# Optimization experiments

Hardware: AMD Instinct MI355X
Metric: run time of the kernel (lower is better)

## Reference

```python
import jax, jax.numpy as jnp
import numpy as np

D_MODEL = 256
NHEAD = 8
AGG = 4
NPE = (832.0, 832.0, 832.0, 832.0)
LAYER_NAMES = ['self', 'cross'] * 4


def layer_norm(x, g, b, eps=1e-5):
    mu = x.mean(-1, keepdims=True)
    var = ((x - mu) ** 2).mean(-1, keepdims=True)
    return (x - mu) * jax.lax.rsqrt(var + eps) * g + b


def rope_tables(h, w, d_model=D_MODEL):
    # i/j positions start at 1 (torch cumsum of ones); npe train/test scaling
    i = (jnp.arange(1, h + 1, dtype=jnp.float32) * (NPE[0] / NPE[2]))[:, None, None]
    j = (jnp.arange(1, w + 1, dtype=jnp.float32) * (NPE[1] / NPE[3]))[None, :, None]
    d4 = d_model // 4
    div = jnp.exp(jnp.arange(d4, dtype=jnp.float32) * (-np.log(10000.0) / d4))

    def interleave(a, bb):
        a = jnp.broadcast_to(a, (h, w, d4))
        bb = jnp.broadcast_to(bb, (h, w, d4))
        return jnp.stack([a, bb], -1).reshape(h, w, 2 * d4)

    sin = interleave(jnp.sin(i * div), jnp.sin(j * div))
    cos = interleave(jnp.cos(i * div), jnp.cos(j * div))
    return jnp.repeat(sin, 2, axis=-1), jnp.repeat(cos, 2, axis=-1)  # [h,w,d_model]


def rotate_half(x):
    xp = x.reshape(*x.shape[:-1], -1, 2)
    return jnp.stack([-xp[..., 1], xp[..., 0]], -1).reshape(*x.shape)


def apply_rope(x, sin, cos):  # x: [b,h,w,c]
    return x * cos + rotate_half(x) * sin


def encoder_layer(x, source, p, use_rope):
    bs, C, H0, W0 = x.shape
    # depthwise-conv aggregation of query features (stride=kernel=AGG, no bias)
    q = jax.lax.conv_general_dilated(
        x, p['agg_w'], (AGG, AGG), 'VALID',
        dimension_numbers=('NCHW', 'OIHW', 'NCHW'), feature_group_count=C)
    q = layer_norm(q.transpose(0, 2, 3, 1), p['ln1_g'], p['ln1_b'])  # [b,h,w,C]
    # max-pool aggregation of source features
    s = jax.lax.reduce_window(source, -jnp.inf, jax.lax.max,
                              (1, 1, AGG, AGG), (1, 1, AGG, AGG), 'VALID')
    s = layer_norm(s.transpose(0, 2, 3, 1), p['ln1_g'], p['ln1_b'])
    query = q @ p['qw']
    key = s @ p['kw']
    value = s @ p['vw']
    if use_rope:
        sin_q, cos_q = rope_tables(query.shape[1], query.shape[2])
        query = apply_rope(query, sin_q, cos_q)
        sin_k, cos_k = rope_tables(key.shape[1], key.shape[2])
        key = apply_rope(key, sin_k, cos_k)
    L = query.shape[1] * query.shape[2]
    S = key.shape[1] * key.shape[2]
    dh = C // NHEAD
    qh = query.reshape(bs, L, NHEAD, dh)
    kh = key.reshape(bs, S, NHEAD, dh)
    vh = value.reshape(bs, S, NHEAD, dh)
    scores = jnp.einsum('blhd,bshd->bhls', qh, kh) / jnp.asarray(dh, qh.dtype) ** 0.5
    attn = jax.nn.softmax(scores, axis=-1)
    m = jnp.einsum('bhls,bshd->blhd', attn, vh).reshape(bs, L, C)
    m = m @ p['mw']  # merge
    m = m.reshape(bs, H0 // AGG, W0 // AGG, C).transpose(0, 3, 1, 2)
    # bilinear upsample x4, align_corners=False (half-pixel, matches jax.image)
    m = jax.image.resize(m, (bs, C, H0, W0), method='bilinear')
    cat = jnp.concatenate([x, m], axis=1).transpose(0, 2, 3, 1)  # [b,H,W,2C]
    h1 = cat @ p['w1']
    h1 = jnp.where(h1 >= 0, h1, 0.01 * h1)  # LeakyReLU
    out = layer_norm(h1 @ p['w2'], p['ln2_g'], p['ln2_b']).transpose(0, 3, 1, 2)
    return x + out


def _forward(feat0, feat1, params):
    for i, name in enumerate(LAYER_NAMES):
        p = {k: v[i] for k, v in params.items()}
        if name == 'self':
            feat0 = encoder_layer(feat0, feat0, p, use_rope=True)
            feat1 = encoder_layer(feat1, feat1, p, use_rope=True)
        else:
            feat0 = encoder_layer(feat0, feat1, p, use_rope=False)
            feat1 = encoder_layer(feat1, feat0, p, use_rope=False)
    return feat0, feat1


def setup_inputs() -> dict:
    key = jax.random.key(0)
    ks = jax.random.split(key, 10)
    C = D_MODEL
    NL = len(LAYER_NAMES)

    def xavier(k, shape, fan_in, fan_out):
        return jax.random.normal(k, shape, jnp.float32) * np.sqrt(2.0 / (fan_in + fan_out))

    return {
        'feat0': jax.random.normal(ks[0], (2, C, 96, 96), jnp.float32),
        'feat1': jax.random.normal(ks[1], (2, C, 96, 96), jnp.float32),
        'agg_w': jax.random.normal(ks[2], (NL, C, 1, AGG, AGG), jnp.float32) * 0.1,
        'qw': xavier(ks[3], (NL, C, C), C, C),
        'kw': xavier(ks[4], (NL, C, C), C, C),
        'vw': xavier(ks[5], (NL, C, C), C, C),
        'mw': xavier(ks[6], (NL, C, C), C, C),
        'w1': xavier(ks[7], (NL, 2 * C, 2 * C), 2 * C, 2 * C),
        'w2': xavier(ks[8], (NL, 2 * C, C), 2 * C, C),
        'ln1_g': jnp.ones((NL, C), jnp.float32),
        'ln1_b': jnp.zeros((NL, C), jnp.float32),
        'ln2_g': jnp.ones((NL, C), jnp.float32),
        'ln2_b': jnp.zeros((NL, C), jnp.float32),
    }


def reference(feat0, feat1, agg_w, qw, kw, vw, mw, w1, w2, ln1_g, ln1_b, ln2_g, ln2_b):
    params = dict(agg_w=agg_w, qw=qw, kw=kw, vw=vw, mw=mw, w1=w1, w2=w2,
                  ln1_g=ln1_g, ln1_b=ln1_b, ln2_g=ln2_g, ln2_b=ln2_b)
    return _forward(feat0, feat1, params)
```

## Files before the change

kernel.cpp:

```cpp
#include <hip/hip_runtime.h>
#include <math.h>

constexpr int BSZ = 2;
constexpr int CH  = 256;
constexpr int IH  = 96, IW = 96;
constexpr int HSS = 24, WSS = 24;
constexpr int SL  = HSS * WSS;
constexpr int NHD = 8, DHD = 32;
constexpr int CH2 = 512;
constexpr int PIX = IH * IW;
constexpr int MFFN = BSZ * PIX;
constexpr long FEATN = (long)BSZ * PIX * CH;

typedef __attribute__((ext_vector_type(8))) short bf16x8;
typedef __attribute__((ext_vector_type(4))) float f32x4;
typedef _Float16 f16;
typedef __attribute__((ext_vector_type(8))) _Float16 f16x8;
typedef __attribute__((ext_vector_type(4))) _Float16 f16x4;


__device__ inline unsigned short f2bf(float f) {
  unsigned u = __float_as_uint(f);
  u += 0x7FFFu + ((u >> 16) & 1u);
  return (unsigned short)(u >> 16);
}
__device__ inline float bf2f(unsigned short u) {
  return __uint_as_float((unsigned)u << 16);
}

__device__ inline void gload16(const void* g, void* l) {
  __builtin_amdgcn_global_load_lds(
      (const __attribute__((address_space(1))) unsigned int*)g,
      (__attribute__((address_space(3))) unsigned int*)l, 16, 0, 0);
}

__global__ __launch_bounds__(256) void k_in_tr(const float* __restrict__ in,
                                               float* __restrict__ out,
                                               unsigned short* __restrict__ outb) {
  __shared__ float t[32][33];
  const int b = blockIdx.z;
  const int p0 = blockIdx.x * 32, c0 = blockIdx.y * 32;
  const int tx = threadIdx.x & 31, ty = threadIdx.x >> 5;
#pragma unroll
  for (int r = 0; r < 4; ++r)
    t[tx][ty + r * 8] = in[((long)b * CH + c0 + ty + r * 8) * PIX + p0 + tx];
  __syncthreads();
#pragma unroll
  for (int r = 0; r < 4; ++r) {
    float v = t[ty + r * 8][tx];
    long row = (long)b * PIX + p0 + ty + r * 8;
    out[row * CH + c0 + tx] = v;
    outb[row * CH + ((c0 + tx) ^ (ty << 3))] = f2bf(v);
  }
}

__global__ __launch_bounds__(256) void k_out_tr(const float* __restrict__ in,
                                                float* __restrict__ out) {
  __shared__ float t[32][33];
  const int b = blockIdx.z;
  const int p0 = blockIdx.x * 32, c0 = blockIdx.y * 32;
  const int tx = threadIdx.x & 31, ty = threadIdx.x >> 5;
#pragma unroll
  for (int r = 0; r < 4; ++r)
    t[ty + r * 8][tx] = in[((long)b * PIX + p0 + ty + r * 8) * CH + c0 + tx];
  __syncthreads();
#pragma unroll
  for (int r = 0; r < 4; ++r)
    out[((long)b * CH + c0 + ty + r * 8) * PIX + p0 + tx] = t[tx][ty + r * 8];
}

__global__ __launch_bounds__(256) void k_wt(const float* __restrict__ W,
                                            unsigned short* __restrict__ WT,
                                            int K, int N, long strideW, long strideT) {
  const long z = blockIdx.z;
  W  += z * strideW;
  WT += z * strideT;
  __shared__ float t[32][33];
  const int n0 = blockIdx.x * 32, k0 = blockIdx.y * 32;
  const int tx = threadIdx.x & 31, ty = threadIdx.x >> 5;
#pragma unroll
  for (int r = 0; r < 4; ++r)
    t[ty + r * 8][tx] = W[(long)(k0 + ty + r * 8) * N + n0 + tx];
  __syncthreads();
#pragma unroll
  for (int r = 0; r < 4; ++r) {
    int n = n0 + ty + r * 8;
    WT[(long)n * K + ((k0 + tx) ^ ((n & 7) << 3))] = f2bf(t[tx][ty + r * 8]);
  }
}

__global__ __launch_bounds__(256) void k_cvt(const float* __restrict__ W,
                                             unsigned short* __restrict__ O) {
  const int i = blockIdx.x;
  const long z = blockIdx.y;
  const int k = threadIdx.x;
  O[(z * CH + i) * CH + (k ^ ((i & 7) << 3))] = f2bf(W[(z * CH + i) * CH + k]);
}

__global__ __launch_bounds__(256) void k_rope_tables(float* __restrict__ sinT,
                                                     float* __restrict__ cosT) {
  int l = blockIdx.x;
  int d = threadIdx.x;
  int ii = l / WSS + 1;
  int jj = l % WSS + 1;
  int kidx = d >> 2;
  bool is_i = ((d >> 1) & 1) == 0;
  float div = expf((float)kidx * -0.14391156831212787f);
  float pos = is_i ? (float)ii : (float)jj;
  float ang = pos * div;
  sinT[(long)l * CH + d] = sinf(ang);
  cosT[(long)l * CH + d] = cosf(ang);
}

__global__ __launch_bounds__(256) void k_agg(const unsigned short* __restrict__ x,
                                             const unsigned short* __restrict__ src,
                                             const float* __restrict__ aggw,
                                             const float* __restrict__ g,
                                             const float* __restrict__ bt,
                                             unsigned short* __restrict__ qln,
                                             unsigned short* __restrict__ sln,
                                             int nb, int same) {
  int bi = blockIdx.x;
  int mode = 0;
  const int nblk = nb * SL / 8;
  if (!same && bi >= nblk) { mode = 1; bi -= nblk; }
  const int doConv = same || (mode == 0);
  const int doPool = same || (mode == 1);
  const int tid = threadIdx.x;
  const int tok = tid >> 5, cg = tid & 31;
  const int lg = bi * 8 + tok;
  const int b = lg / SL, l = lg - b * SL;
  const int i = l / WSS, j = l - i * WSS;
  const unsigned short* in = mode ? src : x;

  float cv[8] = {};
  float mv[8];
#pragma unroll
  for (int e = 0; e < 8; ++e) mv[e] = -INFINITY;
#pragma unroll
  for (int r = 0; r < 4; ++r)
#pragma unroll
    for (int s = 0; s < 4; ++s) {
      const int px = j * 4 + s;
      bf16x8 v = *(const bf16x8*)&in[(((size_t)b * IH + i * 4 + r) * IW + px) * CH +
                                     ((cg * 8) ^ ((px & 7) << 3))];
#pragma unroll
      for (int e = 0; e < 8; ++e) {
        float f = bf2f((unsigned short)v[e]);
        cv[e] += f * aggw[(cg * 8 + e) * 16 + r * 4 + s];
        mv[e] = fmaxf(mv[e], f);
      }
    }
  const size_t orow = (size_t)(b * SL + l) * CH + ((cg * 8) ^ ((l & 7) << 3));
  if (doConv) {
    float s1 = 0.f, s2 = 0.f;
#pragma unroll
    for (int e = 0; e < 8; ++e) { s1 += cv[e]; s2 += cv[e] * cv[e]; }
#pragma unroll
    for (int d = 1; d < 32; d <<= 1) { s1 += __shfl_xor(s1, d); s2 += __shfl_xor(s2, d); }
    float mu = s1 * (1.f / CH);
    float var = s2 * (1.f / CH) - mu * mu;
    float rs = rsqrtf(var + 1e-5f);
    bf16x8 o;
#pragma unroll
    for (int e = 0; e < 8; ++e)
      o[e] = (short)f2bf((cv[e] - mu) * rs * g[cg * 8 + e] + bt[cg * 8 + e]);
    *(bf16x8*)&qln[orow] = o;
  }
  if (doPool) {
    float s1 = 0.f, s2 = 0.f;
#pragma unroll
    for (int e = 0; e < 8; ++e) { s1 += mv[e]; s2 += mv[e] * mv[e]; }
#pragma unroll
    for (int d = 1; d < 32; d <<= 1) { s1 += __shfl_xor(s1, d); s2 += __shfl_xor(s2, d); }
    float mu = s1 * (1.f / CH);
    float var = s2 * (1.f / CH) - mu * mu;
    float rs = rsqrtf(var + 1e-5f);
    bf16x8 o;
#pragma unroll
    for (int e = 0; e < 8; ++e)
      o[e] = (short)f2bf((mv[e] - mu) * rs * g[cg * 8 + e] + bt[cg * 8 + e]);
    *(bf16x8*)&sln[orow] = o;
  }
}

template <int BM, int BN, int OUT>
__global__ __launch_bounds__(256) void k_mm(const unsigned short* __restrict__ A,
                                            const unsigned short* __restrict__ A2,
                                            const unsigned short* __restrict__ Bt,
                                            void* __restrict__ C0, void* __restrict__ C1,
                                            void* __restrict__ C2,
                                            int M, int K, int lda, int ldb,
                                            int koffA, int koffB, int ldc,
                                            const float* __restrict__ sinT,
                                            const float* __restrict__ cosT,
                                            long zsA, long zsB, long zsC) {
  constexpr int BK = 64;
  constexpr int WM = BM / 2, WN = BN / 2;
  constexpr int FM = WM / 16, FN = WN / 16;
  constexpr int RA = BM * BK / 2048, RB = BN * BK / 2048;
  __shared__ unsigned short As[2][BM * BK];
  __shared__ unsigned short Bs[2][BN * BK];
  const int tid = threadIdx.x;
  const int lane = tid & 63, w = tid >> 6;
  const int wr = w >> 1, wc = w & 1;
  const int lq = lane & 15, g = lane >> 4;
  const int sw = (lq & 7) << 3;
  const int bm = blockIdx.x * BM, bn = blockIdx.y * BN;
  const long z = blockIdx.z;
  const unsigned short* Ap = ((OUT == 4 && bn >= CH) ? A2 : A) + z * zsA + koffA;
  const unsigned short* Bp = Bt + z * zsB + koffB;

  auto stA = [&](int buf, int k0) {
#pragma unroll
    for (int i = 0; i < RA; ++i) {
      int e = (i * 256 + tid) * 8;
      gload16(Ap + (size_t)(bm + (e >> 6)) * lda + k0 + (e & 63), &As[buf][e]);
    }
  };
  auto stB = [&](int buf, int k0) {
#pragma unroll
    for (int i = 0; i < RB; ++i) {
      int e = (i * 256 + tid) * 8;
      gload16(Bp + (size_t)(bn + (e >> 6)) * ldb + k0 + (e & 63), &Bs[buf][e]);
    }
  };

  f32x4 acc[FM][FN] = {};
  stA(0, 0); stB(0, 0);
  asm volatile("s_waitcnt vmcnt(0)" ::: "memory");
  __syncthreads();
  int cur = 0;
  for (int k0 = 0; k0 < K; k0 += BK) {
    if (k0 + BK < K) { stA(cur ^ 1, k0 + BK); stB(cur ^ 1, k0 + BK); }
#pragma unroll
    for (int ks = 0; ks < 2; ++ks) {
      const int kx = (ks * 32 + g * 8) ^ sw;
      bf16x8 a[FM], b[FN];
#pragma unroll
      for (int m = 0; m < FM; ++m)
        a[m] = *(const bf16x8*)&As[cur][(wr * WM + m * 16 + lq) * BK + kx];
#pragma unroll
      for (int n = 0; n < FN; ++n)
        b[n] = *(const bf16x8*)&Bs[cur][(wc * WN + n * 16 + lq) * BK + kx];
#pragma unroll
      for (int m = 0; m < FM; ++m)
#pragma unroll
        for (int n = 0; n < FN; ++n)
          acc[m][n] = __builtin_amdgcn_mfma_f32_16x16x32_bf16(a[m], b[n], acc[m][n], 0, 0, 0);
    }
    __syncthreads();
    cur ^= 1;
  }
#pragma unroll
  for (int m = 0; m < FM; ++m) {
    const int rowb = bm + wr * WM + m * 16 + g * 4;
#pragma unroll
    for (int n = 0; n < FN; ++n) {
      const int col = bn + wc * WN + n * 16 + lq;
#pragma unroll
      for (int r = 0; r < 4; ++r) {
        const int row = rowb + r;
        float v = acc[m][n][r];
        if (OUT == 0) {
          ((float*)C0 + z * zsC)[(size_t)row * ldc + col] = v;
        } else if (OUT == 5) {
          ((unsigned short*)C0 + z * zsC)[(size_t)row * ldc + (col ^ ((row & 7) << 3))] = f2bf(v);
        } else {
          const int b = row / SL, s = row - b * SL;
          const int which = col >> 8;
          const int ch = col & 255;
          float vp = __shfl_xor(v, 1);
          if (which < 2 && sinT) {
            float sn = sinT[(size_t)s * CH + ch];
            float cs = cosT[(size_t)s * CH + ch];
            v = ((lane & 1) == 0) ? v * cs - vp * sn : v * cs + vp * sn;
          }
          if (which == 0) v *= 0.17677669529663687f;
          const int h = ch >> 5, d = ch & 31;
          if (which == 0)
            ((f16*)C0)[(((size_t)b * NHD + h) * SL + s) * DHD + d] = (f16)v;
          else if (which == 1)
            ((f16*)C1)[(((size_t)b * NHD + h) * SL + s) * DHD + d] = (f16)v;
          else
            ((f16*)C2)[(((size_t)b * NHD + h) * DHD + d) * SL + s] = (f16)v;
        }
      }
    }
  }
}

__global__ __launch_bounds__(128) void k_attn(const f16* __restrict__ qh,
                                              const f16* __restrict__ kh,
                                              const f16* __restrict__ vt,
                                              unsigned short* __restrict__ msgA) {
  const int bh = blockIdx.x;
  const int b = bh >> 3, h = bh & 7;
  const int tid = threadIdx.x;
  const int sid = tid >> 6;
  const int lane = tid & 63;
  const int lq = lane & 15, g = lane >> 4;
  const int q0 = blockIdx.y * 16;

  const f16x8 qf = *(const f16x8*)&qh[((size_t)bh * SL + q0 + lq) * DHD + g * 8];
  const f16* kbase = kh + (size_t)bh * SL * DHD;
  const f16* vbase = vt + (size_t)bh * DHD * SL;
  const int t0 = sid * 18;

  f16x8 kf = *(const f16x8*)&kbase[((size_t)(t0 * 16 + lq)) * DHD + g * 8];
  f16x4 va = *(const f16x4*)&vbase[(size_t)lq * SL + t0 * 16 + g * 4];
  f16x4 vb = *(const f16x4*)&vbase[(size_t)(16 + lq) * SL + t0 * 16 + g * 4];

  f32x4 o0 = {}, o1 = {};
  float m = -1e30f, l = 0.f;
  for (int tt = 0; tt < 18; ++tt) {
    const int t = t0 + tt;
    const int tn = tt < 17 ? t + 1 : t;
    f16x8 kfn = *(const f16x8*)&kbase[((size_t)(tn * 16 + lq)) * DHD + g * 8];
    f16x4 van = *(const f16x4*)&vbase[(size_t)lq * SL + tn * 16 + g * 4];
    f16x4 vbn = *(const f16x4*)&vbase[(size_t)(16 + lq) * SL + tn * 16 + g * 4];
    f32x4 s = __builtin_amdgcn_mfma_f32_16x16x32_f16(kf, qf, (f32x4){0.f, 0.f, 0.f, 0.f}, 0, 0, 0);
    float tm = fmaxf(fmaxf(s[0], s[1]), fmaxf(s[2], s[3]));
    tm = fmaxf(tm, __shfl_xor(tm, 16));
    tm = fmaxf(tm, __shfl_xor(tm, 32));
    if (__any(tm > m + 5.f)) {
      float mn = fmaxf(m, tm);
      float f = __expf(m - mn);
      o0 *= f; o1 *= f; l *= f; m = mn;
    }
    float e0 = __expf(s[0] - m), e1 = __expf(s[1] - m);
    float e2 = __expf(s[2] - m), e3 = __expf(s[3] - m);
    l += (e0 + e1) + (e2 + e3);
    f16x4 ef = {(f16)e0, (f16)e1, (f16)e2, (f16)e3};
    o0 = __builtin_amdgcn_mfma_f32_16x16x16f16(va, ef, o0, 0, 0, 0);
    o1 = __builtin_amdgcn_mfma_f32_16x16x16f16(vb, ef, o1, 0, 0, 0);
    kf = kfn; va = van; vb = vbn;
  }
  l += __shfl_xor(l, 16);
  l += __shfl_xor(l, 32);

  __shared__ float mS[2][16], lS[2][16];
  __shared__ float oS[2][2][16][17];
  if (g == 0) { mS[sid][lq] = m; lS[sid][lq] = l; }
#pragma unroll
  for (int r = 0; r < 4; ++r) {
    oS[sid][0][g * 4 + r][lq] = o0[r];
    oS[sid][1][g * 4 + r][lq] = o1[r];
  }
  __syncthreads();
  float m0 = mS[0][lq], m1 = mS[1][lq];
  float l0 = lS[0][lq], l1 = lS[1][lq];
  float mn = fmaxf(m0, m1);
  float f0 = __expf(m0 - mn), f1 = __expf(m1 - mn);
  float inv = 1.f / (l0 * f0 + l1 * f1);
  float ov[4];
#pragma unroll
  for (int r = 0; r < 4; ++r)
    ov[r] = (oS[0][sid][g * 4 + r][lq] * f0 + oS[1][sid][g * 4 + r][lq] * f1) * inv;
  const int swz = (lq & 7) << 3;
  unsigned short* mrow = msgA + ((size_t)(b * SL + q0 + lq)) * CH;
  unsigned a0 = f2bf(ov[0]) | ((unsigned)f2bf(ov[1]) << 16);
  unsigned a1 = f2bf(ov[2]) | ((unsigned)f2bf(ov[3]) << 16);
  uint2 u; u.x = a0; u.y = a1;
  *(uint2*)&mrow[(h * DHD + sid * 16 + g * 4) ^ swz] = u;
}

__global__ __launch_bounds__(512) void k_ffn1(const unsigned short* __restrict__ xb,
                                              const unsigned short* __restrict__ w1T,
                                              const float* __restrict__ Z,
                                              unsigned short* __restrict__ h1) {
  constexpr int BM = 128, BN = 128, BK = 64, K = 256;
  constexpr int WM = 32, WN = 64, FM = 2, FN = 4;
  __shared__ unsigned short As[2][BM * BK];
  __shared__ unsigned short Bs[BN * BK];
  const int tid = threadIdx.x;
  const int lane = tid & 63, w = tid >> 6;
  const int wr = w >> 1, wc = w & 1;
  const int lq = lane & 15, g = lane >> 4;
  const int sw = (lq & 7) << 3;
  const int bm = blockIdx.x * BM, bn = blockIdx.y * BN;

  auto stA = [&](int buf, int k0) {
#pragma unroll
    for (int i = 0; i < 2; ++i) {
      int e = (i * 512 + tid) * 8;
      gload16(xb + (size_t)(bm + (e >> 6)) * 256 + k0 + (e & 63), &As[buf][e]);
    }
  };
  auto stB = [&](int k0) {
#pragma unroll
    for (int i = 0; i < 2; ++i) {
      int e = (i * 512 + tid) * 8;
      gload16(w1T + (size_t)(bn + (e >> 6)) * 512 + k0 + (e & 63), &Bs[e]);
    }
  };

  f32x4 acc[FM][FN] = {};
  stA(0, 0); stB(0);
  asm volatile("s_waitcnt vmcnt(0)" ::: "memory");
  __syncthreads();
  int cur = 0;
  for (int k0 = 0; k0 < K; k0 += BK) {
    if (k0 + BK < K) stA(cur ^ 1, k0 + BK);
#pragma unroll
    for (int ks = 0; ks < 2; ++ks) {
      const int kx = (ks * 32 + g * 8) ^ sw;
      bf16x8 a[FM], b[FN];
#pragma unroll
      for (int m = 0; m < FM; ++m)
        a[m] = *(const bf16x8*)&As[cur][(wr * WM + m * 16 + lq) * BK + kx];
#pragma unroll
      for (int n = 0; n < FN; ++n)
        b[n] = *(const bf16x8*)&Bs[(wc * WN + n * 16 + lq) * BK + kx];
#pragma unroll
      for (int m = 0; m < FM; ++m)
#pragma unroll
        for (int n = 0; n < FN; ++n)
          acc[m][n] = __builtin_amdgcn_mfma_f32_16x16x32_bf16(a[m], b[n], acc[m][n], 0, 0, 0);
    }
    __syncthreads();
    if (k0 + BK < K) stB(k0 + BK);
    asm volatile("s_waitcnt vmcnt(0)" ::: "memory");
    __syncthreads();
    cur ^= 1;
  }
#pragma unroll
  for (int m = 0; m < FM; ++m) {
    const int rowb = bm + wr * WM + m * 16 + g * 4;
#pragma unroll
    for (int r = 0; r < 4; ++r) {
      const int row = rowb + r;
      const int b = row / PIX;
      const int p = row - b * PIX;
      const int y = p / IW, xx = p - y * IW;
      float sy = (y + 0.5f) * 0.25f - 0.5f;
      float sx = (xx + 0.5f) * 0.25f - 0.5f;
      int y0 = (int)floorf(sy); float wy = sy - y0;
      int x0 = (int)floorf(sx); float wx = sx - x0;
      int y1 = min(y0 + 1, HSS - 1); y0 = max(y0, 0);
      int x1 = min(x0 + 1, WSS - 1); x0 = max(x0, 0);
      const float* Zb = Z + (size_t)b * SL * CH2;
      const float* z00 = Zb + (size_t)(y0 * WSS + x0) * CH2;
      const float* z01 = Zb + (size_t)(y0 * WSS + x1) * CH2;
      const float* z10 = Zb + (size_t)(y1 * WSS + x0) * CH2;
      const float* z11 = Zb + (size_t)(y1 * WSS + x1) * CH2;
      float w00 = (1.f - wy) * (1.f - wx), w01 = (1.f - wy) * wx;
      float w10 = wy * (1.f - wx), w11 = wy * wx;
      const int rs = (row & 7) << 3;
#pragma unroll
      for (int n = 0; n < FN; ++n) {
        const int col = bn + wc * WN + n * 16 + lq;
        float v = acc[m][n][r] + w00 * z00[col] + w01 * z01[col] +
                  w10 * z10[col] + w11 * z11[col];
        v = v >= 0.f ? v : 0.01f * v;
        h1[(size_t)row * CH2 + (col ^ rs)] = f2bf(v);
      }
    }
  }
}

__global__ __launch_bounds__(512) void k_ffn2(const unsigned short* __restrict__ A,
                                              const unsigned short* __restrict__ Bt,
                                              const float* __restrict__ g2,
                                              const float* __restrict__ b2,
                                              float* __restrict__ x,
                                              unsigned short* __restrict__ xb) {
  constexpr int BM = 64, BK = 64, K = 512;
  __shared__ unsigned short As[2][BM * BK];
  __shared__ unsigned short Bs[256 * BK];
  __shared__ float sS[2][BM], sQ[2][BM];
  __shared__ float gS[256], bS[256];
  const int tid = threadIdx.x;
  const int lane = tid & 63, w = tid >> 6;
  const int wr = w >> 1, wc = w & 1;
  const int lq = lane & 15, g = lane >> 4;
  const int sw = (lq & 7) << 3;
  const int bm = blockIdx.x * BM;
  if (tid < 256) { gS[tid] = g2[tid]; bS[tid] = b2[tid]; }

  auto stA = [&](int buf, int k0) {
    int e = tid * 8;
    gload16(A + (size_t)(bm + (e >> 6)) * K + k0 + (e & 63), &As[buf][e]);
  };
  auto stB = [&](int k0) {
#pragma unroll
    for (int i = 0; i < 4; ++i) {
      int e = (i * 512 + tid) * 8;
      gload16(Bt + (size_t)(e >> 6) * K + k0 + (e & 63), &Bs[e]);
    }
  };

  f32x4 acc[8] = {};
  stA(0, 0); stB(0);
  asm volatile("s_waitcnt vmcnt(0)" ::: "memory");
  __syncthreads();
  int cur = 0;
  for (int k0 = 0; k0 < K; k0 += BK) {
    if (k0 + BK < K) stA(cur ^ 1, k0 + BK);
#pragma unroll
    for (int ks = 0; ks < 2; ++ks) {
      const int kx = (ks * 32 + g * 8) ^ sw;
      bf16x8 a = *(const bf16x8*)&As[cur][(wr * 16 + lq) * BK + kx];
      bf16x8 b[8];
#pragma unroll
      for (int n = 0; n < 8; ++n)
        b[n] = *(const bf16x8*)&Bs[(wc * 128 + n * 16 + lq) * BK + kx];
#pragma unroll
      for (int n = 0; n < 8; ++n)
        acc[n] = __builtin_amdgcn_mfma_f32_16x16x32_bf16(a, b[n], acc[n], 0, 0, 0);
    }
    __syncthreads();
    if (k0 + BK < K) stB(k0 + BK);
    asm volatile("s_waitcnt vmcnt(0)" ::: "memory");
    __syncthreads();
    cur ^= 1;
  }
#pragma unroll
  for (int r = 0; r < 4; ++r) {
    float s1 = 0.f, s2 = 0.f;
#pragma unroll
    for (int n = 0; n < 8; ++n) {
      float v = acc[n][r];
      s1 += v; s2 += v * v;
    }
#pragma unroll
    for (int d = 1; d < 16; d <<= 1) {
      s1 += __shfl_xor(s1, d);
      s2 += __shfl_xor(s2, d);
    }
    if (lq == 0) {
      int row = wr * 16 + g * 4 + r;
      sS[wc][row] = s1; sQ[wc][row] = s2;
    }
  }
  __syncthreads();
#pragma unroll
  for (int r = 0; r < 4; ++r) {
    int row = wr * 16 + g * 4 + r;
    float mu = (sS[0][row] + sS[1][row]) * (1.f / CH);
    float var = (sQ[0][row] + sQ[1][row]) * (1.f / CH) - mu * mu;
    float rs = rsqrtf(var + 1e-5f);
    size_t gr = (size_t)(bm + row) * CH;
    const int swr = ((bm + row) & 7) << 3;
#pragma unroll
    for (int n = 0; n < 8; ++n) {
      int col = wc * 128 + n * 16 + lq;
      float o = (acc[n][r] - mu) * rs * gS[col] + bS[col];
      float nx = x[gr + col] + o;
      x[gr + col] = nx;
      xb[gr + (col ^ swr)] = f2bf(nx);
    }
  }
}

struct LayerP {
  const float *aggw, *g1, *b1, *g2, *b2;
  const unsigned short *qkvT, *w1T, *w2T, *wcT;
};

struct Bufs {
  unsigned short *qln, *sln, *msgA, *h1, *xb;
  f16 *qh, *kh, *vt;
  float *Zbuf, *f;
  const float *sinT, *cosT;
};

static void attn_part(long xoff, long soff, const LayerP& p, bool rope, int nb,
                      const Bufs& B, hipStream_t stream) {
  const int M = nb * SL;
  const int same = (xoff == soff) ? 1 : 0;
  const int nblk = (same ? 1 : 2) * nb * SL / 8;
  k_agg<<<dim3(nblk), 256, 0, stream>>>(B.xb + xoff, B.xb + soff, p.aggw,
                                        p.g1, p.b1, B.qln, B.sln, nb, same);
  const float* sT = rope ? B.sinT : nullptr;
  const float* cT = rope ? B.cosT : nullptr;
  k_mm<32, 64, 4><<<dim3(M / 32, 12), 256, 0, stream>>>(
      B.qln, B.sln, p.qkvT, B.qh, B.kh, B.vt, M, CH, CH, CH, 0, 0, 0, sT, cT, 0, 0, 0);
  k_attn<<<dim3(nb * NHD, 36), 128, 0, stream>>>(B.qh, B.kh, B.vt, B.msgA);
  k_mm<64, 64, 0><<<dim3(M / 64, 8), 256, 0, stream>>>(
      B.msgA, nullptr, p.wcT, B.Zbuf, nullptr, nullptr, M, CH, CH, CH, 0, 0, CH2,
      nullptr, nullptr, 0, 0, 0);
}

static void ffn_part(int fi, int nf, const float* Zs, const LayerP& p, const Bufs& B,
                     hipStream_t stream) {
  const int M = nf * MFFN;
  k_ffn1<<<dim3(M / 128, CH2 / 128), 512, 0, stream>>>(B.xb + (long)fi * FEATN, p.w1T, Zs, B.h1);
  k_ffn2<<<dim3(M / 64), 512, 0, stream>>>(B.h1, p.w2T, p.g2, p.b2,
                                           B.f + (long)fi * FEATN, B.xb + (long)fi * FEATN);
}

extern "C" void kernel_launch(void* const* d_in, const int* in_sizes, int n_in,
                              void* d_out, int out_size, void* d_ws, size_t ws_size,
                              hipStream_t stream) {
  const float* in_f0 = (const float*)d_in[0];
  const float* in_f1 = (const float*)d_in[1];
  const float* aggw  = (const float*)d_in[2];
  const float* qw    = (const float*)d_in[3];
  const float* kw    = (const float*)d_in[4];
  const float* vw    = (const float*)d_in[5];
  const float* mw    = (const float*)d_in[6];
  const float* w1    = (const float*)d_in[7];
  const float* w2    = (const float*)d_in[8];
  const float* g1    = (const float*)d_in[9];
  const float* b1    = (const float*)d_in[10];
  const float* g2    = (const float*)d_in[11];
  const float* b2    = (const float*)d_in[12];
  (void)in_sizes; (void)n_in; (void)out_size; (void)ws_size;

  char* cur = (char*)d_ws;
  auto alloc = [&](size_t bytes) { void* p = cur; cur += (bytes + 255) & ~(size_t)255; return p; };
  float*          f    = (float*)alloc((size_t)2 * FEATN * 4);
  unsigned short* xb   = (unsigned short*)alloc((size_t)2 * FEATN * 2);
  unsigned short* h1   = (unsigned short*)alloc((size_t)2 * MFFN * CH2 * 2);
  float*          Zbuf = (float*)alloc((size_t)4 * SL * CH2 * 4);
  unsigned short* msgA = (unsigned short*)alloc((size_t)4 * SL * CH * 2);
  unsigned short* qln  = (unsigned short*)alloc((size_t)4 * SL * CH * 2);
  unsigned short* sln  = (unsigned short*)alloc((size_t)4 * SL * CH * 2);
  f16* qh = (f16*)alloc((size_t)4 * NHD * SL * DHD * 2);
  f16* kh = (f16*)alloc((size_t)4 * NHD * SL * DHD * 2);
  f16* vt = (f16*)alloc((size_t)4 * NHD * SL * DHD * 2);
  float* sinT = (float*)alloc((size_t)SL * CH * 4);
  float* cosT = (float*)alloc((size_t)SL * CH * 4);
  unsigned short* qkvT = (unsigned short*)alloc((size_t)8 * 3 * CH * CH * 2);
  unsigned short* mwB  = (unsigned short*)alloc((size_t)8 * CH * CH * 2);
  unsigned short* w1T  = (unsigned short*)alloc((size_t)8 * CH2 * CH2 * 2);
  unsigned short* w2T  = (unsigned short*)alloc((size_t)8 * CH * CH2 * 2);
  unsigned short* wcT  = (unsigned short*)alloc((size_t)8 * CH2 * CH * 2);

  k_in_tr<<<dim3(PIX / 32, CH / 32, BSZ), 256, 0, stream>>>(in_f0, f, xb);
  k_in_tr<<<dim3(PIX / 32, CH / 32, BSZ), 256, 0, stream>>>(in_f1, f + FEATN, xb + FEATN);
  k_rope_tables<<<dim3(SL), 256, 0, stream>>>(sinT, cosT);
  k_wt<<<dim3(CH / 32, CH / 32, 8), 256, 0, stream>>>(qw, qkvT, CH, CH, (long)CH * CH, (long)3 * CH * CH);
  k_wt<<<dim3(CH / 32, CH / 32, 8), 256, 0, stream>>>(kw, qkvT + (size_t)CH * CH, CH, CH, (long)CH * CH, (long)3 * CH * CH);
  k_wt<<<dim3(CH / 32, CH / 32, 8), 256, 0, stream>>>(vw, qkvT + (size_t)2 * CH * CH, CH, CH, (long)CH * CH, (long)3 * CH * CH);
  k_cvt<<<dim3(CH, 8), 256, 0, stream>>>(mw, mwB);
  k_wt<<<dim3(CH2 / 32, CH2 / 32, 8), 256, 0, stream>>>(w1, w1T, CH2, CH2, (long)CH2 * CH2, (long)CH2 * CH2);
  k_wt<<<dim3(CH / 32, CH2 / 32, 8), 256, 0, stream>>>(w2, w2T, CH2, CH, (long)CH2 * CH, (long)CH * CH2);
  k_mm<64, 64, 5><<<dim3(CH2 / 64, CH / 64, 8), 256, 0, stream>>>(
      w1T, nullptr, mwB, wcT, nullptr, nullptr, CH2, CH, CH2, CH, 256, 0, CH,
      nullptr, nullptr, (long)CH2 * CH2, (long)CH * CH, (long)CH2 * CH);

  Bufs B{qln, sln, msgA, h1, xb, qh, kh, vt, Zbuf, f, sinT, cosT};

  for (int i = 0; i < 8; ++i) {
    LayerP p{aggw + (long)i * CH * 16,
             g1 + i * CH, b1 + i * CH, g2 + i * CH, b2 + i * CH,
             qkvT + (long)i * 3 * CH * CH,
             w1T + (long)i * CH2 * CH2, w2T + (long)i * CH * CH2,
             wcT + (long)i * CH2 * CH};
    if ((i & 1) == 0) {
      attn_part(0, 0, p, true, 4, B, stream);
      ffn_part(0, 2, Zbuf, p, B, stream);
    } else {
      attn_part(0, FEATN, p, false, 2, B, stream);
      ffn_part(0, 1, Zbuf, p, B, stream);
      attn_part(FEATN, 0, p, false, 2, B, stream);
      ffn_part(1, 1, Zbuf, p, B, stream);
    }
  }

  float* outp = (float*)d_out;
  k_out_tr<<<dim3(PIX / 32, CH / 32, BSZ), 256, 0, stream>>>(f, outp);
  k_out_tr<<<dim3(PIX / 32, CH / 32, BSZ), 256, 0, stream>>>(f + FEATN, outp + FEATN);
}
```

Before: 1.067 ms.

## Switch storage and MFMA to fp16 and drop the fp32 residual copy

Converts every bf16 buffer and weight to fp16 and uses fp16 MFMA. The separate fp32 residual stream is removed, so the feature map lives only as a swizzled fp16 buffer that FFN2 updates in place, and the output transpose reads from it. The aim is to cut memory traffic per layer, since FFN2 no longer reads and writes the fp32 residual plus a bf16 copy. k_agg is also relaunched with 64-thread blocks. The cost is that the residual accumulates in fp16 across eight layers, which risks precision loss or overflow compared with an fp32 residual.

New measurement: 975.4 us. 8.6% less time.

```diff
diff --git a/kernel.cpp b/kernel.cpp
--- a/kernel.cpp
+++ b/kernel.cpp
@@ -12,22 +12,12 @@
 constexpr int MFFN = BSZ * PIX;
 constexpr long FEATN = (long)BSZ * PIX * CH;
 
-typedef __attribute__((ext_vector_type(8))) short bf16x8;
 typedef __attribute__((ext_vector_type(4))) float f32x4;
 typedef _Float16 f16;
 typedef __attribute__((ext_vector_type(8))) _Float16 f16x8;
 typedef __attribute__((ext_vector_type(4))) _Float16 f16x4;
 
 
-__device__ inline unsigned short f2bf(float f) {
-  unsigned u = __float_as_uint(f);
-  u += 0x7FFFu + ((u >> 16) & 1u);
-  return (unsigned short)(u >> 16);
-}
-__device__ inline float bf2f(unsigned short u) {
-  return __uint_as_float((unsigned)u << 16);
-}
-
 __device__ inline void gload16(const void* g, void* l) {
   __builtin_amdgcn_global_load_lds(
       (const __attribute__((address_space(1))) unsigned int*)g,
@@ -35,8 +25,7 @@
 }
 
 __global__ __launch_bounds__(256) void k_in_tr(const float* __restrict__ in,
-                                               float* __restrict__ out,
-                                               unsigned short* __restrict__ outb) {
+                                               f16* __restrict__ outh) {
   __shared__ float t[32][33];
   const int b = blockIdx.z;
   const int p0 = blockIdx.x * 32, c0 = blockIdx.y * 32;
@@ -47,14 +36,12 @@
   __syncthreads();
 #pragma unroll
   for (int r = 0; r < 4; ++r) {
-    float v = t[ty + r * 8][tx];
     long row = (long)b * PIX + p0 + ty + r * 8;
-    out[row * CH + c0 + tx] = v;
-    outb[row * CH + ((c0 + tx) ^ (ty << 3))] = f2bf(v);
-  }
-}
-
-__global__ __launch_bounds__(256) void k_out_tr(const float* __restrict__ in,
+    outh[row * CH + ((c0 + tx) ^ (ty << 3))] = (f16)t[ty + r * 8][tx];
+  }
+}
+
+__global__ __launch_bounds__(256) void k_out_tr(const f16* __restrict__ in,
                                                 float* __restrict__ out) {
   __shared__ float t[32][33];
   const int b = blockIdx.z;
@@ -62,7 +49,8 @@
   const int tx = threadIdx.x & 31, ty = threadIdx.x >> 5;
 #pragma unroll
   for (int r = 0; r < 4; ++r)
-    t[ty + r * 8][tx] = in[((long)b * PIX + p0 + ty + r * 8) * CH + c0 + tx];
+    t[ty + r * 8][tx] =
+        (float)in[((long)b * PIX + p0 + ty + r * 8) * CH + ((c0 + tx) ^ (ty << 3))];
   __syncthreads();
 #pragma unroll
   for (int r = 0; r < 4; ++r)
@@ -70,7 +58,7 @@
 }
 
 __global__ __launch_bounds__(256) void k_wt(const float* __restrict__ W,
-                                            unsigned short* __restrict__ WT,
+                                            f16* __restrict__ WT,
                                             int K, int N, long strideW, long strideT) {
   const long z = blockIdx.z;
   W  += z * strideW;
@@ -85,16 +73,16 @@
 #pragma unroll
   for (int r = 0; r < 4; ++r) {
     int n = n0 + ty + r * 8;
-    WT[(long)n * K + ((k0 + tx) ^ ((n & 7) << 3))] = f2bf(t[tx][ty + r * 8]);
+    WT[(long)n * K + ((k0 + tx) ^ ((n & 7) << 3))] = (f16)t[tx][ty + r * 8];
   }
 }
 
 __global__ __launch_bounds__(256) void k_cvt(const float* __restrict__ W,
-                                             unsigned short* __restrict__ O) {
+                                             f16* __restrict__ O) {
   const int i = blockIdx.x;
   const long z = blockIdx.y;
   const int k = threadIdx.x;
-  O[(z * CH + i) * CH + (k ^ ((i & 7) << 3))] = f2bf(W[(z * CH + i) * CH + k]);
+  O[(z * CH + i) * CH + (k ^ ((i & 7) << 3))] = (f16)W[(z * CH + i) * CH + k];
 }
 
 __global__ __launch_bounds__(256) void k_rope_tables(float* __restrict__ sinT,
@@ -112,26 +100,26 @@
   cosT[(long)l * CH + d] = cosf(ang);
 }
 
-__global__ __launch_bounds__(256) void k_agg(const unsigned short* __restrict__ x,
-                                             const unsigned short* __restrict__ src,
-                                             const float* __restrict__ aggw,
-                                             const float* __restrict__ g,
-                                             const float* __restrict__ bt,
-                                             unsigned short* __restrict__ qln,
-                                             unsigned short* __restrict__ sln,
-                                             int nb, int same) {
+__global__ __launch_bounds__(64) void k_agg(const f16* __restrict__ x,
+                                            const f16* __restrict__ src,
+                                            const float* __restrict__ aggw,
+                                            const float* __restrict__ g,
+                                            const float* __restrict__ bt,
+                                            f16* __restrict__ qln,
+                                            f16* __restrict__ sln,
+                                            int nb, int same) {
   int bi = blockIdx.x;
   int mode = 0;
-  const int nblk = nb * SL / 8;
+  const int nblk = nb * SL / 2;
   if (!same && bi >= nblk) { mode = 1; bi -= nblk; }
   const int doConv = same || (mode == 0);
   const int doPool = same || (mode == 1);
   const int tid = threadIdx.x;
   const int tok = tid >> 5, cg = tid & 31;
-  const int lg = bi * 8 + tok;
+  const int lg = bi * 2 + tok;
   const int b = lg / SL, l = lg - b * SL;
   const int i = l / WSS, j = l - i * WSS;
-  const unsigned short* in = mode ? src : x;
+  const f16* in = mode ? src : x;
 
   float cv[8] = {};
   float mv[8];
@@ -142,11 +130,11 @@
 #pragma unroll
     for (int s = 0; s < 4; ++s) {
       const int px = j * 4 + s;
-      bf16x8 v = *(const bf16x8*)&in[(((size_t)b * IH + i * 4 + r) * IW + px) * CH +
-                                     ((cg * 8) ^ ((px & 7) << 3))];
+      f16x8 v = *(const f16x8*)&in[(((size_t)b * IH + i * 4 + r) * IW + px) * CH +
+                                   ((cg * 8) ^ ((px & 7) << 3))];
 #pragma unroll
       for (int e = 0; e < 8; ++e) {
-        float f = bf2f((unsigned short)v[e]);
+        float f = (float)v[e];
         cv[e] += f * aggw[(cg * 8 + e) * 16 + r * 4 + s];
         mv[e] = fmaxf(mv[e], f);
       }
@@ -161,11 +149,11 @@
     float mu = s1 * (1.f / CH);
     float var = s2 * (1.f / CH) - mu * mu;
     float rs = rsqrtf(var + 1e-5f);
-    bf16x8 o;
+    f16x8 o;
 #pragma unroll
     for (int e = 0; e < 8; ++e)
-      o[e] = (short)f2bf((cv[e] - mu) * rs * g[cg * 8 + e] + bt[cg * 8 + e]);
-    *(bf16x8*)&qln[orow] = o;
+      o[e] = (f16)((cv[e] - mu) * rs * g[cg * 8 + e] + bt[cg * 8 + e]);
+    *(f16x8*)&qln[orow] = o;
   }
   if (doPool) {
     float s1 = 0.f, s2 = 0.f;
@@ -176,18 +164,18 @@
     float mu = s1 * (1.f / CH);
     float var = s2 * (1.f / CH) - mu * mu;
     float rs = rsqrtf(var + 1e-5f);
-    bf16x8 o;
+    f16x8 o;
 #pragma unroll
     for (int e = 0; e < 8; ++e)
-      o[e] = (short)f2bf((mv[e] - mu) * rs * g[cg * 8 + e] + bt[cg * 8 + e]);
-    *(bf16x8*)&sln[orow] = o;
+      o[e] = (f16)((mv[e] - mu) * rs * g[cg * 8 + e] + bt[cg * 8 + e]);
+    *(f16x8*)&sln[orow] = o;
   }
 }
 
 template <int BM, int BN, int OUT>
-__global__ __launch_bounds__(256) void k_mm(const unsigned short* __restrict__ A,
-                                            const unsigned short* __restrict__ A2,
-                                            const unsigned short* __restrict__ Bt,
+__global__ __launch_bounds__(256) void k_mm(const f16* __restrict__ A,
+                                            const f16* __restrict__ A2,
+                                            const f16* __restrict__ Bt,
                                             void* __restrict__ C0, void* __restrict__ C1,
                                             void* __restrict__ C2,
                                             int M, int K, int lda, int ldb,
@@ -199,8 +187,8 @@
   constexpr int WM = BM / 2, WN = BN / 2;
   constexpr int FM = WM / 16, FN = WN / 16;
   constexpr int RA = BM * BK / 2048, RB = BN * BK / 2048;
-  __shared__ unsigned short As[2][BM * BK];
-  __shared__ unsigned short Bs[2][BN * BK];
+  __shared__ f16 As[2][BM * BK];
+  __shared__ f16 Bs[2][BN * BK];
   const int tid = threadIdx.x;
   const int lane = tid & 63, w = tid >> 6;
   const int wr = w >> 1, wc = w & 1;
@@ -208,8 +196,8 @@
   const int sw = (lq & 7) << 3;
   const int bm = blockIdx.x * BM, bn = blockIdx.y * BN;
   const long z = blockIdx.z;
-  const unsigned short* Ap = ((OUT == 4 && bn >= CH) ? A2 : A) + z * zsA + koffA;
-  const unsigned short* Bp = Bt + z * zsB + koffB;
+  const f16* Ap = ((OUT == 4 && bn >= CH) ? A2 : A) + z * zsA + koffA;
+  const f16* Bp = Bt + z * zsB + koffB;
 
   auto stA = [&](int buf, int k0) {
 #pragma unroll
@@ -236,18 +224,18 @@
 #pragma unroll
     for (int ks = 0; ks < 2; ++ks) {
       const int kx = (ks * 32 + g * 8) ^ sw;
-      bf16x8 a[FM], b[FN];
+      f16x8 a[FM], b[FN];
 #pragma unroll
       for (int m = 0; m < FM; ++m)
-        a[m] = *(const bf16x8*)&As[cur][(wr * WM + m * 16 + lq) * BK + kx];
+        a[m] = *(const f16x8*)&As[cur][(wr * WM + m * 16 + lq) * BK + kx];
 #pragma unroll
       for (int n = 0; n < FN; ++n)
-        b[n] = *(const bf16x8*)&Bs[cur][(wc * WN + n * 16 + lq) * BK + kx];
+        b[n] = *(const f16x8*)&Bs[cur][(wc * WN + n * 16 + lq) * BK + kx];
 #pragma unroll
       for (int m = 0; m < FM; ++m)
 #pragma unroll
         for (int n = 0; n < FN; ++n)
-          acc[m][n] = __builtin_amdgcn_mfma_f32_16x16x32_bf16(a[m], b[n], acc[m][n], 0, 0, 0);
+          acc[m][n] = __builtin_amdgcn_mfma_f32_16x16x32_f16(a[m], b[n], acc[m][n], 0, 0, 0);
     }
     __syncthreads();
     cur ^= 1;
@@ -265,7 +253,7 @@
         if (OUT == 0) {
           ((float*)C0 + z * zsC)[(size_t)row * ldc + col] = v;
         } else if (OUT == 5) {
-          ((unsigned short*)C0 + z * zsC)[(size_t)row * ldc + (col ^ ((row & 7) << 3))] = f2bf(v);
+          ((f16*)C0 + z * zsC)[(size_t)row * ldc + (col ^ ((row & 7) << 3))] = (f16)v;
         } else {
           const int b = row / SL, s = row - b * SL;
           const int which = col >> 8;
@@ -293,7 +281,7 @@
 __global__ __launch_bounds__(128) void k_attn(const f16* __restrict__ qh,
                                               const f16* __restrict__ kh,
                                               const f16* __restrict__ vt,
-                                              unsigned short* __restrict__ msgA) {
+                                              f16* __restrict__ msgA) {
   const int bh = blockIdx.x;
   const int b = bh >> 3, h = bh & 7;
   const int tid = threadIdx.x;
@@ -353,26 +341,23 @@
   float mn = fmaxf(m0, m1);
   float f0 = __expf(m0 - mn), f1 = __expf(m1 - mn);
   float inv = 1.f / (l0 * f0 + l1 * f1);
-  float ov[4];
+  f16x4 ov;
 #pragma unroll
   for (int r = 0; r < 4; ++r)
-    ov[r] = (oS[0][sid][g * 4 + r][lq] * f0 + oS[1][sid][g * 4 + r][lq] * f1) * inv;
+    ov[r] = (f16)((oS[0][sid][g * 4 + r][lq] * f0 + oS[1][sid][g * 4 + r][lq] * f1) * inv);
   const int swz = (lq & 7) << 3;
-  unsigned short* mrow = msgA + ((size_t)(b * SL + q0 + lq)) * CH;
-  unsigned a0 = f2bf(ov[0]) | ((unsigned)f2bf(ov[1]) << 16);
-  unsigned a1 = f2bf(ov[2]) | ((unsigned)f2bf(ov[3]) << 16);
-  uint2 u; u.x = a0; u.y = a1;
-  *(uint2*)&mrow[(h * DHD + sid * 16 + g * 4) ^ swz] = u;
-}
-
-__global__ __launch_bounds__(512) void k_ffn1(const unsigned short* __restrict__ xb,
-                                              const unsigned short* __restrict__ w1T,
+  f16* mrow = msgA + ((size_t)(b * SL + q0 + lq)) * CH;
+  *(f16x4*)&mrow[(h * DHD + sid * 16 + g * 4) ^ swz] = ov;
+}
+
+__global__ __launch_bounds__(512) void k_ffn1(const f16* __restrict__ xh,
+                                              const f16* __restrict__ w1T,
                                               const float* __restrict__ Z,
-                                              unsigned short* __restrict__ h1) {
+                                              f16* __restrict__ h1) {
   constexpr int BM = 128, BN = 128, BK = 64, K = 256;
   constexpr int WM = 32, WN = 64, FM = 2, FN = 4;
-  __shared__ unsigned short As[2][BM * BK];
-  __shared__ unsigned short Bs[BN * BK];
+  __shared__ f16 As[2][BM * BK];
+  __shared__ f16 Bs[BN * BK];
   const int tid = threadIdx.x;
   const int lane = tid & 63, w = tid >> 6;
   const int wr = w >> 1, wc = w & 1;
@@ -384,7 +369,7 @@
 #pragma unroll
     for (int i = 0; i < 2; ++i) {
       int e = (i * 512 + tid) * 8;
-      gload16(xb + (size_t)(bm + (e >> 6)) * 256 + k0 + (e & 63), &As[buf][e]);
+      gload16(xh + (size_t)(bm + (e >> 6)) * 256 + k0 + (e & 63), &As[buf][e]);
     }
   };
   auto stB = [&](int k0) {
@@ -405,18 +390,18 @@
 #pragma unroll
     for (int ks = 0; ks < 2; ++ks) {
       const int kx = (ks * 32 + g * 8) ^ sw;
-      bf16x8 a[FM], b[FN];
+      f16x8 a[FM], b[FN];
 #pragma unroll
       for (int m = 0; m < FM; ++m)
-        a[m] = *(const bf16x8*)&As[cur][(wr * WM + m * 16 + lq) * BK + kx];
+        a[m] = *(const f16x8*)&As[cur][(wr * WM + m * 16 + lq) * BK + kx];
 #pragma unroll
       for (int n = 0; n < FN; ++n)
-        b[n] = *(const bf16x8*)&Bs[(wc * WN + n * 16 + lq) * BK + kx];
+        b[n] = *(const f16x8*)&Bs[(wc * WN + n * 16 + lq) * BK + kx];
 #pragma unroll
       for (int m = 0; m < FM; ++m)
 #pragma unroll
         for (int n = 0; n < FN; ++n)
-          acc[m][n] = __builtin_amdgcn_mfma_f32_16x16x32_bf16(a[m], b[n], acc[m][n], 0, 0, 0);
+          acc[m][n] = __builtin_amdgcn_mfma_f32_16x16x32_f16(a[m], b[n], acc[m][n], 0, 0, 0);
     }
     __syncthreads();
     if (k0 + BK < K) stB(k0 + BK);
@@ -453,21 +438,20 @@
         float v = acc[m][n][r] + w00 * z00[col] + w01 * z01[col] +
                   w10 * z10[col] + w11 * z11[col];
         v = v >= 0.f ? v : 0.01f * v;
-        h1[(size_t)row * CH2 + (col ^ rs)] = f2bf(v);
+        h1[(size_t)row * CH2 + (col ^ rs)] = (f16)v;
       }
     }
   }
 }
 
-__global__ __launch_bounds__(512) void k_ffn2(const unsigned short* __restrict__ A,
-                                              const unsigned short* __restrict__ Bt,
+__global__ __launch_bounds__(512) void k_ffn2(const f16* __restrict__ A,
+                                              const f16* __restrict__ Bt,
                                               const float* __restrict__ g2,
                                               const float* __restrict__ b2,
-                                              float* __restrict__ x,
-                                              unsigned short* __restrict__ xb) {
+                                              f16* __restrict__ xh) {
   constexpr int BM = 64, BK = 64, K = 512;
-  __shared__ unsigned short As[2][BM * BK];
-  __shared__ unsigned short Bs[256 * BK];
+  __shared__ f16 As[2][BM * BK];
+  __shared__ f16 Bs[256 * BK];
   __shared__ float sS[2][BM], sQ[2][BM];
   __shared__ float gS[256], bS[256];
   const int tid = threadIdx.x;
@@ -500,14 +484,14 @@
 #pragma unroll
     for (int ks = 0; ks < 2; ++ks) {
       const int kx = (ks * 32 + g * 8) ^ sw;
-      bf16x8 a = *(const bf16x8*)&As[cur][(wr * 16 + lq) * BK + kx];
-      bf16x8 b[8];
+      f16x8 a = *(const f16x8*)&As[cur][(wr * 16 + lq) * BK + kx];
+      f16x8 b[8];
 #pragma unroll
       for (int n = 0; n < 8; ++n)
-        b[n] = *(const bf16x8*)&Bs[(wc * 128 + n * 16 + lq) * BK + kx];
+        b[n] = *(const f16x8*)&Bs[(wc * 128 + n * 16 + lq) * BK + kx];
 #pragma unroll
       for (int n = 0; n < 8; ++n)
-        acc[n] = __builtin_amdgcn_mfma_f32_16x16x32_bf16(a, b[n], acc[n], 0, 0, 0);
+        acc[n] = __builtin_amdgcn_mfma_f32_16x16x32_f16(a, b[n], acc[n], 0, 0, 0);
     }
     __syncthreads();
     if (k0 + BK < K) stB(k0 + BK);
@@ -540,28 +524,27 @@
     float mu = (sS[0][row] + sS[1][row]) * (1.f / CH);
     float var = (sQ[0][row] + sQ[1][row]) * (1.f / CH) - mu * mu;
     float rs = rsqrtf(var + 1e-5f);
-    size_t gr = (size_t)(bm + row) * CH;
+    f16* base = xh + (size_t)(bm + row) * CH;
     const int swr = ((bm + row) & 7) << 3;
 #pragma unroll
     for (int n = 0; n < 8; ++n) {
       int col = wc * 128 + n * 16 + lq;
       float o = (acc[n][r] - mu) * rs * gS[col] + bS[col];
-      float nx = x[gr + col] + o;
-      x[gr + col] = nx;
-      xb[gr + (col ^ swr)] = f2bf(nx);
+      int ci = col ^ swr;
+      base[ci] = (f16)((float)base[ci] + o);
     }
   }
 }
 
 struct LayerP {
   const float *aggw, *g1, *b1, *g2, *b2;
-  const unsigned short *qkvT, *w1T, *w2T, *wcT;
+  const f16 *qkvT, *w1T, *w2T, *wcT;
 };
 
 struct Bufs {
-  unsigned short *qln, *sln, *msgA, *h1, *xb;
+  f16 *qln, *sln, *msgA, *h1, *xh;
   f16 *qh, *kh, *vt;
-  float *Zbuf, *f;
+  float *Zbuf;
   const float *sinT, *cosT;
 };
 
@@ -569,9 +552,9 @@
                       const Bufs& B, hipStream_t stream) {
   const int M = nb * SL;
   const int same = (xoff == soff) ? 1 : 0;
-  const int nblk = (same ? 1 : 2) * nb * SL / 8;
-  k_agg<<<dim3(nblk), 256, 0, stream>>>(B.xb + xoff, B.xb + soff, p.aggw,
-                                        p.g1, p.b1, B.qln, B.sln, nb, same);
+  const int nblk = (same ? 1 : 2) * nb * SL / 2;
+  k_agg<<<dim3(nblk), 64, 0, stream>>>(B.xh + xoff, B.xh + soff, p.aggw,
+                                       p.g1, p.b1, B.qln, B.sln, nb, same);
   const float* sT = rope ? B.sinT : nullptr;
   const float* cT = rope ? B.cosT : nullptr;
   k_mm<32, 64, 4><<<dim3(M / 32, 12), 256, 0, stream>>>(
@@ -585,9 +568,9 @@
 static void ffn_part(int fi, int nf, const float* Zs, const LayerP& p, const Bufs& B,
                      hipStream_t stream) {
   const int M = nf * MFFN;
-  k_ffn1<<<dim3(M / 128, CH2 / 128), 512, 0, stream>>>(B.xb + (long)fi * FEATN, p.w1T, Zs, B.h1);
+  k_ffn1<<<dim3(M / 128, CH2 / 128), 512, 0, stream>>>(B.xh + (long)fi * FEATN, p.w1T, Zs, B.h1);
   k_ffn2<<<dim3(M / 64), 512, 0, stream>>>(B.h1, p.w2T, p.g2, p.b2,
-                                           B.f + (long)fi * FEATN, B.xb + (long)fi * FEATN);
+                                           B.xh + (long)fi * FEATN);
 }
 
 extern "C" void kernel_launch(void* const* d_in, const int* in_sizes, int n_in,
@@ -610,38 +593,37 @@
 
   char* cur = (char*)d_ws;
   auto alloc = [&](size_t bytes) { void* p = cur; cur += (bytes + 255) & ~(size_t)255; return p; };
-  float*          f    = (float*)alloc((size_t)2 * FEATN * 4);
-  unsigned short* xb   = (unsigned short*)alloc((size_t)2 * FEATN * 2);
-  unsigned short* h1   = (unsigned short*)alloc((size_t)2 * MFFN * CH2 * 2);
-  float*          Zbuf = (float*)alloc((size_t)4 * SL * CH2 * 4);
-  unsigned short* msgA = (unsigned short*)alloc((size_t)4 * SL * CH * 2);
-  unsigned short* qln  = (unsigned short*)alloc((size_t)4 * SL * CH * 2);
-  unsigned short* sln  = (unsigned short*)alloc((size_t)4 * SL * CH * 2);
+  f16*   xh   = (f16*)alloc((size_t)2 * FEATN * 2);
+  f16*   h1   = (f16*)alloc((size_t)2 * MFFN * CH2 * 2);
+  float* Zbuf = (float*)alloc((size_t)4 * SL * CH2 * 4);
+  f16*   msgA = (f16*)alloc((size_t)4 * SL * CH * 2);
+  f16*   qln  = (f16*)alloc((size_t)4 * SL * CH * 2);
+  f16*   sln  = (f16*)alloc((size_t)4 * SL * CH * 2);
   f16* qh = (f16*)alloc((size_t)4 * NHD * SL * DHD * 2);
   f16* kh = (f16*)alloc((size_t)4 * NHD * SL * DHD * 2);
   f16* vt = (f16*)alloc((size_t)4 * NHD * SL * DHD * 2);
   float* sinT = (float*)alloc((size_t)SL * CH * 4);
   float* cosT = (float*)alloc((size_t)SL * CH * 4);
-  unsigned short* qkvT = (unsigned short*)alloc((size_t)8 * 3 * CH * CH * 2);
-  unsigned short* mwB  = (unsigned short*)alloc((size_t)8 * CH * CH * 2);
-  unsigned short* w1T  = (unsigned short*)alloc((size_t)8 * CH2 * CH2 * 2);
-  unsigned short* w2T  = (unsigned short*)alloc((size_t)8 * CH * CH2 * 2);
-  unsigned short* wcT  = (unsigned short*)alloc((size_t)8 * CH2 * CH * 2);
-
-  k_in_tr<<<dim3(PIX / 32, CH / 32, BSZ), 256, 0, stream>>>(in_f0, f, xb);
-  k_in_tr<<<dim3(PIX / 32, CH / 32, BSZ), 256, 0, stream>>>(in_f1, f + FEATN, xb + FEATN);
+  f16* qkvT = (f16*)alloc((size_t)8 * 3 * CH * CH * 2);
+  f16* mwH  = (f16*)alloc((size_t)8 * CH * CH * 2);
+  f16* w1T  = (f16*)alloc((size_t)8 * CH2 * CH2 * 2);
+  f16* w2T  = (f16*)alloc((size_t)8 * CH * CH2 * 2);
+  f16* wcT  = (f16*)alloc((size_t)8 * CH2 * CH * 2);
+
+  k_in_tr<<<dim3(PIX / 32, CH / 32, BSZ), 256, 0, stream>>>(in_f0, xh);
+  k_in_tr<<<dim3(PIX / 32, CH / 32, BSZ), 256, 0, stream>>>(in_f1, xh + FEATN);
   k_rope_tables<<<dim3(SL), 256, 0, stream>>>(sinT, cosT);
   k_wt<<<dim3(CH / 32, CH / 32, 8), 256, 0, stream>>>(qw, qkvT, CH, CH, (long)CH * CH, (long)3 * CH * CH);
   k_wt<<<dim3(CH / 32, CH / 32, 8), 256, 0, stream>>>(kw, qkvT + (size_t)CH * CH, CH, CH, (long)CH * CH, (long)3 * CH * CH);
   k_wt<<<dim3(CH / 32, CH / 32, 8), 256, 0, stream>>>(vw, qkvT + (size_t)2 * CH * CH, CH, CH, (long)CH * CH, (long)3 * CH * CH);
-  k_cvt<<<dim3(CH, 8), 256, 0, stream>>>(mw, mwB);
+  k_cvt<<<dim3(CH, 8), 256, 0, stream>>>(mw, mwH);
   k_wt<<<dim3(CH2 / 32, CH2 / 32, 8), 256, 0, stream>>>(w1, w1T, CH2, CH2, (long)CH2 * CH2, (long)CH2 * CH2);
   k_wt<<<dim3(CH / 32, CH2 / 32, 8), 256, 0, stream>>>(w2, w2T, CH2, CH, (long)CH2 * CH, (long)CH * CH2);
   k_mm<64, 64, 5><<<dim3(CH2 / 64, CH / 64, 8), 256, 0, stream>>>(
-      w1T, nullptr, mwB, wcT, nullptr, nullptr, CH2, CH, CH2, CH, 256, 0, CH,
+      w1T, nullptr, mwH, wcT, nullptr, nullptr, CH2, CH, CH2, CH, 256, 0, CH,
       nullptr, nullptr, (long)CH2 * CH2, (long)CH * CH, (long)CH2 * CH);
 
-  Bufs B{qln, sln, msgA, h1, xb, qh, kh, vt, Zbuf, f, sinT, cosT};
+  Bufs B{qln, sln, msgA, h1, xh, qh, kh, vt, Zbuf, sinT, cosT};
 
   for (int i = 0; i < 8; ++i) {
     LayerP p{aggw + (long)i * CH * 16,
@@ -661,6 +643,6 @@
   }
 
   float* outp = (float*)d_out;
-  k_out_tr<<<dim3(PIX / 32, CH / 32, BSZ), 256, 0, stream>>>(f, outp);
-  k_out_tr<<<dim3(PIX / 32, CH / 32, BSZ), 256, 0, stream>>>(f + FEATN, outp + FEATN);
-}
+  k_out_tr<<<dim3(PIX / 32, CH / 32, BSZ), 256, 0, stream>>>(xh, outp);
+  k_out_tr<<<dim3(PIX / 32, CH / 32, BSZ), 256, 0, stream>>>(xh + FEATN, outp + FEATN);
+}
```
